# Kernel optimization log

Measured on AMD Instinct MI355X. Metric: run time of the kernel, lower is better.

The kernel has to match this reference:

```python
import jax, jax.numpy as jnp
import numpy as np

N_NODES = 50000


def setup_inputs() -> dict:
    key = jax.random.key(0)
    k1, k2, k3, k4, k5 = jax.random.split(key, 5)
    N, E, D_IN, D_OUT = N_NODES, 800000, 128, 128
    features = jax.random.normal(k1, (N, D_IN), dtype=jnp.float32)
    src = jax.random.randint(k2, (E,), 0, N, dtype=jnp.int32)
    dst = jax.random.randint(k3, (E,), 0, N, dtype=jnp.int32)
    # Kaiming-ish init for linear weights
    W_self = jax.random.normal(k4, (D_IN, D_OUT), dtype=jnp.float32) / np.sqrt(D_IN)
    W_neigh = jax.random.normal(k5, (D_IN, D_OUT), dtype=jnp.float32) / np.sqrt(D_IN)
    b = jnp.zeros((D_OUT,), dtype=jnp.float32)
    return {"features": features, "src": src, "dst": dst,
            "W_self": W_self, "W_neigh": W_neigh, "b": b}


def reference(features, src, dst, W_self, W_neigh, b):
    # DGL SAGEConv with 'mean' aggregator:
    #   h_neigh[v] = mean_{(u->v) in E} features[u]   (0 if in-degree 0)
    #   out = features @ W_self + h_neigh @ W_neigh + b
    N = features.shape[0]
    # gather source features along edges, then segment-sum into destinations
    neigh_sum = jax.ops.segment_sum(features[src], dst, num_segments=N)  # [N, D]
    deg = jax.ops.segment_sum(jnp.ones_like(dst, dtype=features.dtype), dst,
                              num_segments=N)  # [N]
    h_neigh = neigh_sum / jnp.maximum(deg, 1.0)[:, None]
    return features @ W_self + h_neigh @ W_neigh + b
```

## Files before the change

### kernel.cpp

```cpp
#include <hip/hip_runtime.h>

#define D 128
#define EC 1024
#define BSH 8
#define CAP 5120
#define HPAD 136
#define CSTR 16

typedef __attribute__((ext_vector_type(8))) short bf16x8;
typedef __attribute__((ext_vector_type(4))) float f32x4;

__device__ __forceinline__ unsigned short f2bf(float f) {
    union { float f; unsigned int u; } c;
    c.f = f;
    unsigned int lsb = (c.u >> 16) & 1u;
    c.u += 0x7fffu + lsb;
    return (unsigned short)(c.u >> 16);
}

__device__ __forceinline__ float bf_lo(unsigned int x) {
    union { unsigned int u; float f; } c;
    c.u = x << 16;
    return c.f;
}
__device__ __forceinline__ float bf_hi(unsigned int x) {
    union { unsigned int u; float f; } c;
    c.u = x & 0xffff0000u;
    return c.f;
}

__global__ __launch_bounds__(256) void prep_kernel(const float* __restrict__ feat,
                                                   unsigned short* __restrict__ fb,
                                                   const float* __restrict__ Ws,
                                                   const float* __restrict__ Wn,
                                                   unsigned short* __restrict__ Wfrag,
                                                   int* __restrict__ bin_cursor,
                                                   int castB, int n8) {
    int bid = blockIdx.x;
    int t   = threadIdx.x;
    if (bid < castB) {
        int i = bid * 256 + t;
        if (i >= n8) return;
        const float4* s = (const float4*)(feat + (size_t)i * 8);
        float4 a = s[0];
        float4 b = s[1];
        unsigned short pk[8];
        pk[0] = f2bf(a.x); pk[1] = f2bf(a.y); pk[2] = f2bf(a.z); pk[3] = f2bf(a.w);
        pk[4] = f2bf(b.x); pk[5] = f2bf(b.y); pk[6] = f2bf(b.z); pk[7] = f2bf(b.w);
        *(bf16x8*)(fb + (size_t)i * 8) = *(const bf16x8*)pk;
    } else if (bid < castB + 16) {
        int tid = (bid - castB) * 256 + t;
        int l  = tid & 63;
        int ks = (tid >> 6) & 7;
        int nt = tid >> 9;
        int n  = nt * 16 + (l & 15);
        int kb = ks * 32 + (l >> 4) * 8;
        unsigned short pk[8];
#pragma unroll
        for (int j = 0; j < 8; ++j) {
            int k = kb + j;
            float w = (k < 128) ? Ws[k * D + n] : Wn[(k - 128) * D + n];
            pk[j] = f2bf(w);
        }
        *(bf16x8*)(Wfrag + (size_t)tid * 8) = *(const bf16x8*)pk;
    } else {
#pragma unroll
        for (int j = 0; j < CSTR; ++j)
            bin_cursor[j * 256 + t] = 0;
    }
}

__global__ __launch_bounds__(256) void binscatter_kernel(const int* __restrict__ src,
                                                         const int* __restrict__ dst,
                                                         int* __restrict__ bin_cursor,
                                                         unsigned int* __restrict__ ebuf,
                                                         int E, int NB) {
    __shared__ int cnt[256];
    __shared__ int basev[256];
    __shared__ int cur[256];
    int t = threadIdx.x;
    cnt[t] = 0;
    cur[t] = 0;
    __syncthreads();
    int base = blockIdx.x * EC;
    int dr[EC / 256];
#pragma unroll
    for (int i = 0; i < EC / 256; ++i) {
        int e = base + i * 256 + t;
        dr[i] = (e < E) ? dst[e] : -1;
        if (dr[i] >= 0) atomicAdd(&cnt[dr[i] >> BSH], 1);
    }
    __syncthreads();
    if (t < NB && cnt[t]) basev[t] = atomicAdd(&bin_cursor[t * CSTR], cnt[t]);
    __syncthreads();
#pragma unroll
    for (int i = 0; i < EC / 256; ++i) {
        int e = base + i * 256 + t;
        if (dr[i] >= 0) {
            int d = dr[i];
            int b = d >> BSH;
            int loc = basev[b] + atomicAdd(&cur[b], 1);
            if (loc < CAP)
                ebuf[(size_t)b * CAP + loc] =
                    (unsigned int)src[e] | ((unsigned int)(d & ((1 << BSH) - 1)) << 16);
        }
    }
}

__global__ __launch_bounds__(1024) void csrbin_kernel(const unsigned int* __restrict__ ebuf,
                                                      const int* __restrict__ bin_cursor,
                                                      int* __restrict__ rs_g,
                                                      int* __restrict__ deg_g,
                                                      unsigned short* __restrict__ bucket,
                                                      int N) {
    __shared__ int degL[256];
    __shared__ int scn[256];
    __shared__ int cur[256];
    int b = blockIdx.x;
    int t = threadIdx.x;
    int cntb = bin_cursor[b * CSTR];
    if (cntb > CAP) cntb = CAP;
    int s  = b * CAP;
    int e2 = s + cntb;

    if (t < 256) { degL[t] = 0; cur[t] = 0; }
    __syncthreads();
    for (int i = s + t; i < e2; i += 1024)
        atomicAdd(&degL[(ebuf[i] >> 16) & 255], 1);
    __syncthreads();

    if (t < 256) scn[t] = degL[t];
    __syncthreads();
    for (int off = 1; off < 256; off <<= 1) {
        int add = 0;
        if (t < 256 && t >= off) add = scn[t - off];
        __syncthreads();
        if (t < 256) scn[t] += add;
        __syncthreads();
    }

    for (int i = s + t; i < e2; i += 1024) {
        unsigned int p = ebuf[i];
        int dl = (p >> 16) & 255;
        int sl = atomicAdd(&cur[dl], 1);
        bucket[s + (scn[dl] - degL[dl]) + sl] = (unsigned short)(p & 0xffffu);
    }

    if (t < 256) {
        int node = (b << BSH) + t;
        if (node < N) {
            rs_g[node]  = s + scn[t] - degL[t];
            deg_g[node] = degL[t];
        }
    }
}

__global__ __launch_bounds__(512) void gather_mfma_kernel(
        const unsigned short* __restrict__ fb,
        const unsigned short* __restrict__ bucket,
        const int* __restrict__ rs,
        const int* __restrict__ deg,
        const unsigned short* __restrict__ Wfrag,
        const float* __restrict__ bias,
        float* __restrict__ out, int N) {
    __shared__ unsigned short hL[64 * HPAD];

    int t    = threadIdx.x;
    int w    = t >> 6;
    int lane = t & 63;
    int lo16 = lane & 15;
    int quad = lane >> 4;
    int g    = quad;
    int c    = lo16;
    int v0   = blockIdx.x * 64;

    int nidx = v0 + w * 8 + (lane & 7);
    int ncl  = (nidx < N) ? nidx : N - 1;
    int dv   = deg[ncl];
    int bv   = rs[ncl];

    for (int nn = 0; nn < 8; ++nn) {
        int node = v0 + w * 8 + nn;
        int d    = __shfl(dv, nn);
        int base = __shfl(bv, nn);

        float acc[8];
#pragma unroll
        for (int j = 0; j < 8; ++j) acc[j] = 0.f;

        if (node < N) {
            int u0 = (g < d)      ? (int)bucket[base + g]      : 0;
            int u1 = (g + 4 < d)  ? (int)bucket[base + g + 4]  : 0;
            int u2 = (g + 8 < d)  ? (int)bucket[base + g + 8]  : 0;
            int u3 = (g + 12 < d) ? (int)bucket[base + g + 12] : 0;
            for (int i = g; i < d; i += 16) {
                int n0 = (i + 16 < d) ? (int)bucket[base + i + 16] : 0;
                int n1 = (i + 20 < d) ? (int)bucket[base + i + 20] : 0;
                int n2 = (i + 24 < d) ? (int)bucket[base + i + 24] : 0;
                int n3 = (i + 28 < d) ? (int)bucket[base + i + 28] : 0;
                bool b1 = (i + 4 < d), b2 = (i + 8 < d), b3 = (i + 12 < d);
                uint4 x0 = *(const uint4*)(fb + (size_t)u0 * D + c * 8);
                uint4 x1, x2, x3;
                if (b1) x1 = *(const uint4*)(fb + (size_t)u1 * D + c * 8);
                if (b2) x2 = *(const uint4*)(fb + (size_t)u2 * D + c * 8);
                if (b3) x3 = *(const uint4*)(fb + (size_t)u3 * D + c * 8);
                acc[0] += bf_lo(x0.x); acc[1] += bf_hi(x0.x);
                acc[2] += bf_lo(x0.y); acc[3] += bf_hi(x0.y);
                acc[4] += bf_lo(x0.z); acc[5] += bf_hi(x0.z);
                acc[6] += bf_lo(x0.w); acc[7] += bf_hi(x0.w);
                if (b1) {
                    acc[0] += bf_lo(x1.x); acc[1] += bf_hi(x1.x);
                    acc[2] += bf_lo(x1.y); acc[3] += bf_hi(x1.y);
                    acc[4] += bf_lo(x1.z); acc[5] += bf_hi(x1.z);
                    acc[6] += bf_lo(x1.w); acc[7] += bf_hi(x1.w);
                }
                if (b2) {
                    acc[0] += bf_lo(x2.x); acc[1] += bf_hi(x2.x);
                    acc[2] += bf_lo(x2.y); acc[3] += bf_hi(x2.y);
                    acc[4] += bf_lo(x2.z); acc[5] += bf_hi(x2.z);
                    acc[6] += bf_lo(x2.w); acc[7] += bf_hi(x2.w);
                }
                if (b3) {
                    acc[0] += bf_lo(x3.x); acc[1] += bf_hi(x3.x);
                    acc[2] += bf_lo(x3.y); acc[3] += bf_hi(x3.y);
                    acc[4] += bf_lo(x3.z); acc[5] += bf_hi(x3.z);
                    acc[6] += bf_lo(x3.w); acc[7] += bf_hi(x3.w);
                }
                u0 = n0; u1 = n1; u2 = n2; u3 = n3;
            }
        }

#pragma unroll
        for (int j = 0; j < 8; ++j) {
            acc[j] += __shfl_xor(acc[j], 16);
            acc[j] += __shfl_xor(acc[j], 32);
        }

        if (g == 0) {
            float inv = (node < N && d > 0) ? 1.0f / (float)d : 0.0f;
            unsigned short pk[8];
#pragma unroll
            for (int j = 0; j < 8; ++j) pk[j] = f2bf(acc[j] * inv);
            *(bf16x8*)&hL[(w * 8 + nn) * HPAD + c * 8] = *(const bf16x8*)pk;
        }
    }
    __syncthreads();

    int wr = w & 3;
    int wc = w >> 2;
    int rowA = v0 + wr * 16 + lo16;
    if (rowA > N - 1) rowA = N - 1;
    int lrow = wr * 16 + lo16;

    f32x4 accO[4];
#pragma unroll
    for (int ntl = 0; ntl < 4; ++ntl) accO[ntl] = (f32x4){0.f, 0.f, 0.f, 0.f};

#pragma unroll
    for (int ks = 0; ks < 8; ++ks) {
        bf16x8 a;
        if (ks < 4)
            a = *(const bf16x8*)(fb + (size_t)rowA * D + ks * 32 + quad * 8);
        else
            a = *(const bf16x8*)&hL[lrow * HPAD + (ks - 4) * 32 + quad * 8];
        const unsigned short* wp = Wfrag + ((size_t)ks * 64 + lane) * 8;
#pragma unroll
        for (int ntl = 0; ntl < 4; ++ntl) {
            int nt = wc * 4 + ntl;
            bf16x8 b = *(const bf16x8*)(wp + (size_t)nt * 4096);
            accO[ntl] = __builtin_amdgcn_mfma_f32_16x16x32_bf16(a, b, accO[ntl], 0, 0, 0);
        }
    }

#pragma unroll
    for (int ntl = 0; ntl < 4; ++ntl) {
        int n = (wc * 4 + ntl) * 16 + lo16;
        float bvl = bias[n];
#pragma unroll
        for (int r = 0; r < 4; ++r) {
            int row = v0 + wr * 16 + quad * 4 + r;
            if (row < N) out[(size_t)row * D + n] = accO[ntl][r] + bvl;
        }
    }
}

extern "C" void kernel_launch(void* const* d_in, const int* in_sizes, int n_in,
                              void* d_out, int out_size, void* d_ws, size_t ws_size,
                              hipStream_t stream) {
    const float* feat = (const float*)d_in[0];
    const int*   src  = (const int*)d_in[1];
    const int*   dst  = (const int*)d_in[2];
    const float* Ws   = (const float*)d_in[3];
    const float* Wn   = (const float*)d_in[4];
    const float* bias = (const float*)d_in[5];
    float*       out  = (float*)d_out;

    const int N  = in_sizes[0] / D;
    const int E  = in_sizes[1];
    const int NB = (N + (1 << BSH) - 1) >> BSH;
    const int nchunk = (E + EC - 1) / EC;
    const int castB  = (N * D / 8 + 255) / 256;

    int* bin_cursor = (int*)d_ws;
    int* rs         = bin_cursor + 256 * CSTR;
    int* deg        = rs + N;
    unsigned int* ebuf = (unsigned int*)(deg + N);
    unsigned short* bucket = (unsigned short*)(ebuf + (size_t)NB * CAP);
    size_t short_count = (size_t)NB * CAP;
    short_count = (short_count + 7) & ~(size_t)7;
    unsigned short* fb    = bucket + short_count;
    unsigned short* Wfrag = fb + (size_t)N * D;

    prep_kernel<<<castB + 17, 256, 0, stream>>>(feat, fb, Ws, Wn, Wfrag, bin_cursor,
                                                castB, N * D / 8);
    binscatter_kernel<<<nchunk, 256, 0, stream>>>(src, dst, bin_cursor, ebuf, E, NB);
    csrbin_kernel<<<NB, 1024, 0, stream>>>(ebuf, bin_cursor, rs, deg, bucket, N);
    gather_mfma_kernel<<<(N + 63) / 64, 512, 0, stream>>>(fb, bucket, rs, deg, Wfrag,
                                                          bias, out, N);
}
```

Measured before the change: 174.6 us.

## Assign one node per 16-lane group in gather and halve block size

Restructures the gather phase so each 16-lane group owns a whole destination node and loads up to 16 neighbor rows at once. Neighbor indices are broadcast with shuffles, which removes the cross-quad shuffle reduction and gives more loads in flight per lane. The block shrinks to 256 threads, so each wave now computes all 8 output column tiles of the MFMA projection. The trade-off is higher register pressure from the 16-entry row buffer and the 8 accumulators, which may lower occupancy.

```diff
diff --git a/kernel.cpp b/kernel.cpp
--- a/kernel.cpp
+++ b/kernel.cpp
@@ -155,7 +155,7 @@
     }
 }
 
-__global__ __launch_bounds__(512) void gather_mfma_kernel(
+__global__ __launch_bounds__(256) void gather_mfma_kernel(
         const unsigned short* __restrict__ fb,
         const unsigned short* __restrict__ bucket,
         const int* __restrict__ rs,
@@ -166,95 +166,62 @@
     __shared__ unsigned short hL[64 * HPAD];
 
     int t    = threadIdx.x;
+    int lane = t & 63;
+    int c    = t & 15;
+    int G    = t >> 4;
+    int v0   = blockIdx.x * 64;
+
+    for (int it = 0; it < 4; ++it) {
+        int node = v0 + it * 16 + G;
+        int ncl  = (node < N) ? node : N - 1;
+        int d    = deg[ncl];
+        int base = rs[ncl];
+        if (node >= N) d = 0;
+
+        float acc[8];
+#pragma unroll
+        for (int j = 0; j < 8; ++j) acc[j] = 0.f;
+
+        for (int i0 = 0; i0 < d; i0 += 16) {
+            int m = d - i0; if (m > 16) m = 16;
+            int uc = (c < m) ? (int)bucket[base + i0 + c] : 0;
+            uint4 rr[16];
+#pragma unroll
+            for (int e = 0; e < 16; ++e) {
+                if (e < m) {
+                    int ue = __shfl(uc, (lane & 48) + e);
+                    rr[e] = *(const uint4*)(fb + (size_t)ue * D + c * 8);
+                }
+            }
+#pragma unroll
+            for (int e = 0; e < 16; ++e) {
+                if (e < m) {
+                    acc[0] += bf_lo(rr[e].x); acc[1] += bf_hi(rr[e].x);
+                    acc[2] += bf_lo(rr[e].y); acc[3] += bf_hi(rr[e].y);
+                    acc[4] += bf_lo(rr[e].z); acc[5] += bf_hi(rr[e].z);
+                    acc[6] += bf_lo(rr[e].w); acc[7] += bf_hi(rr[e].w);
+                }
+            }
+        }
+
+        float inv = (d > 0) ? 1.0f / (float)d : 0.0f;
+        unsigned short pk[8];
+#pragma unroll
+        for (int j = 0; j < 8; ++j) pk[j] = f2bf(acc[j] * inv);
+        *(bf16x8*)&hL[(it * 16 + G) * HPAD + c * 8] = *(const bf16x8*)pk;
+    }
+    __syncthreads();
+
     int w    = t >> 6;
-    int lane = t & 63;
     int lo16 = lane & 15;
     int quad = lane >> 4;
-    int g    = quad;
-    int c    = lo16;
-    int v0   = blockIdx.x * 64;
-
-    int nidx = v0 + w * 8 + (lane & 7);
-    int ncl  = (nidx < N) ? nidx : N - 1;
-    int dv   = deg[ncl];
-    int bv   = rs[ncl];
-
-    for (int nn = 0; nn < 8; ++nn) {
-        int node = v0 + w * 8 + nn;
-        int d    = __shfl(dv, nn);
-        int base = __shfl(bv, nn);
-
-        float acc[8];
-#pragma unroll
-        for (int j = 0; j < 8; ++j) acc[j] = 0.f;
-
-        if (node < N) {
-            int u0 = (g < d)      ? (int)bucket[base + g]      : 0;
-            int u1 = (g + 4 < d)  ? (int)bucket[base + g + 4]  : 0;
-            int u2 = (g + 8 < d)  ? (int)bucket[base + g + 8]  : 0;
-            int u3 = (g + 12 < d) ? (int)bucket[base + g + 12] : 0;
-            for (int i = g; i < d; i += 16) {
-                int n0 = (i + 16 < d) ? (int)bucket[base + i + 16] : 0;
-                int n1 = (i + 20 < d) ? (int)bucket[base + i + 20] : 0;
-                int n2 = (i + 24 < d) ? (int)bucket[base + i + 24] : 0;
-                int n3 = (i + 28 < d) ? (int)bucket[base + i + 28] : 0;
-                bool b1 = (i + 4 < d), b2 = (i + 8 < d), b3 = (i + 12 < d);
-                uint4 x0 = *(const uint4*)(fb + (size_t)u0 * D + c * 8);
-                uint4 x1, x2, x3;
-                if (b1) x1 = *(const uint4*)(fb + (size_t)u1 * D + c * 8);
-                if (b2) x2 = *(const uint4*)(fb + (size_t)u2 * D + c * 8);
-                if (b3) x3 = *(const uint4*)(fb + (size_t)u3 * D + c * 8);
-                acc[0] += bf_lo(x0.x); acc[1] += bf_hi(x0.x);
-                acc[2] += bf_lo(x0.y); acc[3] += bf_hi(x0.y);
-                acc[4] += bf_lo(x0.z); acc[5] += bf_hi(x0.z);
-                acc[6] += bf_lo(x0.w); acc[7] += bf_hi(x0.w);
-                if (b1) {
-                    acc[0] += bf_lo(x1.x); acc[1] += bf_hi(x1.x);
-                    acc[2] += bf_lo(x1.y); acc[3] += bf_hi(x1.y);
-                    acc[4] += bf_lo(x1.z); acc[5] += bf_hi(x1.z);
-                    acc[6] += bf_lo(x1.w); acc[7] += bf_hi(x1.w);
-                }
-                if (b2) {
-                    acc[0] += bf_lo(x2.x); acc[1] += bf_hi(x2.x);
-                    acc[2] += bf_lo(x2.y); acc[3] += bf_hi(x2.y);
-                    acc[4] += bf_lo(x2.z); acc[5] += bf_hi(x2.z);
-                    acc[6] += bf_lo(x2.w); acc[7] += bf_hi(x2.w);
-                }
-                if (b3) {
-                    acc[0] += bf_lo(x3.x); acc[1] += bf_hi(x3.x);
-                    acc[2] += bf_lo(x3.y); acc[3] += bf_hi(x3.y);
-                    acc[4] += bf_lo(x3.z); acc[5] += bf_hi(x3.z);
-                    acc[6] += bf_lo(x3.w); acc[7] += bf_hi(x3.w);
-                }
-                u0 = n0; u1 = n1; u2 = n2; u3 = n3;
-            }
-        }
-
-#pragma unroll
-        for (int j = 0; j < 8; ++j) {
-            acc[j] += __shfl_xor(acc[j], 16);
-            acc[j] += __shfl_xor(acc[j], 32);
-        }
-
-        if (g == 0) {
-            float inv = (node < N && d > 0) ? 1.0f / (float)d : 0.0f;
-            unsigned short pk[8];
-#pragma unroll
-            for (int j = 0; j < 8; ++j) pk[j] = f2bf(acc[j] * inv);
-            *(bf16x8*)&hL[(w * 8 + nn) * HPAD + c * 8] = *(const bf16x8*)pk;
-        }
-    }
-    __syncthreads();
-
-    int wr = w & 3;
-    int wc = w >> 2;
-    int rowA = v0 + wr * 16 + lo16;
+    int rowA = v0 + w * 16 + lo16;
     if (rowA > N - 1) rowA = N - 1;
-    int lrow = wr * 16 + lo16;
-
-    f32x4 accO[4];
-#pragma unroll
-    for (int ntl = 0; ntl < 4; ++ntl) accO[ntl] = (f32x4){0.f, 0.f, 0.f, 0.f};
+    int lrow = w * 16 + lo16;
+
+    f32x4 accO[8];
+#pragma unroll
+    for (int nt = 0; nt < 8; ++nt) accO[nt] = (f32x4){0.f, 0.f, 0.f, 0.f};
 
 #pragma unroll
     for (int ks = 0; ks < 8; ++ks) {
@@ -265,21 +232,20 @@
             a = *(const bf16x8*)&hL[lrow * HPAD + (ks - 4) * 32 + quad * 8];
         const unsigned short* wp = Wfrag + ((size_t)ks * 64 + lane) * 8;
 #pragma unroll
-        for (int ntl = 0; ntl < 4; ++ntl) {
-            int nt = wc * 4 + ntl;
+        for (int nt = 0; nt < 8; ++nt) {
             bf16x8 b = *(const bf16x8*)(wp + (size_t)nt * 4096);
-            accO[ntl] = __builtin_amdgcn_mfma_f32_16x16x32_bf16(a, b, accO[ntl], 0, 0, 0);
-        }
-    }
-
-#pragma unroll
-    for (int ntl = 0; ntl < 4; ++ntl) {
-        int n = (wc * 4 + ntl) * 16 + lo16;
+            accO[nt] = __builtin_amdgcn_mfma_f32_16x16x32_bf16(a, b, accO[nt], 0, 0, 0);
+        }
+    }
+
+#pragma unroll
+    for (int nt = 0; nt < 8; ++nt) {
+        int n = nt * 16 + lo16;
         float bvl = bias[n];
 #pragma unroll
         for (int r = 0; r < 4; ++r) {
-            int row = v0 + wr * 16 + quad * 4 + r;
-            if (row < N) out[(size_t)row * D + n] = accO[ntl][r] + bvl;
+            int row = v0 + w * 16 + quad * 4 + r;
+            if (row < N) out[(size_t)row * D + n] = accO[nt][r] + bvl;
         }
     }
 }
@@ -315,6 +281,6 @@
                                                 castB, N * D / 8);
     binscatter_kernel<<<nchunk, 256, 0, stream>>>(src, dst, bin_cursor, ebuf, E, NB);
     csrbin_kernel<<<NB, 1024, 0, stream>>>(ebuf, bin_cursor, rs, deg, bucket, N);
-    gather_mfma_kernel<<<(N + 63) / 64, 512, 0, stream>>>(fb, bucket, rs, deg, Wfrag,
+    gather_mfma_kernel<<<(N + 63) / 64, 256, 0, stream>>>(fb, bucket, rs, deg, Wfrag,
                                                           bias, out, N);
 }
```

New measurement: 216.0 us. +23.7%, slower.
